# Kernel tuning notes

Hardware: AMD Instinct MI355X
Metric: run time of the kernel (lower is better)

The kernel has to match this reference:

```python
import jax, jax.numpy as jnp
import numpy as np

DIM = 1024
EXP = 4
B, S = 4, 4096


def setup_inputs() -> dict:
    key = jax.random.key(0)
    ks = jax.random.split(key, 20)
    d, h = DIM, DIM * EXP
    sc = 1.0 / np.sqrt(d)
    inp = {
        "x": jax.random.normal(ks[0], (B, S, d), dtype=jnp.float32),
        # attention linears, stored [in, out] so y = x @ W + b
        "wq": jax.random.normal(ks[1], (d, d), jnp.float32) * sc,
        "bq": jnp.zeros((d,), jnp.float32),
        "wk": jax.random.normal(ks[2], (d, d), jnp.float32) * sc,
        "bk": jnp.zeros((d,), jnp.float32),
        "wv": jax.random.normal(ks[3], (d, d), jnp.float32) * sc,
        "bv": jnp.zeros((d,), jnp.float32),
        "wo": jax.random.normal(ks[4], (d, d), jnp.float32) * sc,
        "bo": jnp.zeros((d,), jnp.float32),
        # FFN
        "w1": jax.random.normal(ks[5], (d, h), jnp.float32) * sc,
        "b1": jnp.zeros((h,), jnp.float32),
        "w2": jax.random.normal(ks[6], (h, d), jnp.float32) * (1.0 / np.sqrt(h)),
        "b2": jnp.zeros((d,), jnp.float32),
        # LayerNorms
        "g1": jnp.ones((d,), jnp.float32),
        "beta1": jnp.zeros((d,), jnp.float32),
        "g2": jnp.ones((d,), jnp.float32),
        "beta2": jnp.zeros((d,), jnp.float32),
    }
    return inp


def _layernorm(x, g, b, eps=1e-5):
    mu = jnp.mean(x, axis=-1, keepdims=True)
    var = jnp.mean(jnp.square(x - mu), axis=-1, keepdims=True)
    return (x - mu) * jax.lax.rsqrt(var + eps) * g + b


def _block(x, wq, bq, wk, bk, wv, bv, wo, bo, w1, b1, w2, b2, g1, beta1, g2, beta2):
    d = x.shape[-1]
    # attention sub-block (single head, full [B,S,S] scores as in source)
    h = _layernorm(x, g1, beta1)
    q = h @ wq + bq
    k = h @ wk + bk
    v = h @ wv + bv
    scores = jnp.einsum("bsd,btd->bst", q, k) / jnp.sqrt(jnp.asarray(d, x.dtype))
    attn = jax.nn.softmax(scores, axis=-1)
    a = jnp.einsum("bst,btd->bsd", attn, v) @ wo + bo
    x = x + a
    # FFN sub-block (exact GELU, matching torch nn.GELU default)
    h2 = _layernorm(x, g2, beta2)
    f = jax.nn.gelu(h2 @ w1 + b1, approximate=False) @ w2 + b2
    return x + f


def reference(x, wq, bq, wk, bk, wv, bv, wo, bo, w1, b1, w2, b2, g1, beta1, g2, beta2):
    return _block(x, wq, bq, wk, bk, wv, bv, wo, bo, w1, b1, w2, b2, g1, beta1, g2, beta2)
```

## Files before the change

kernel.cpp:

```cpp
#include <hip/hip_runtime.h>
#include <hip/hip_bf16.h>
#include <cstdint>

typedef __bf16 bf16;
typedef __bf16 bf16x8 __attribute__((ext_vector_type(8)));
typedef __bf16 bf16x4 __attribute__((ext_vector_type(4)));
typedef float f32x4 __attribute__((ext_vector_type(4)));

#define DEV __device__ __forceinline__

DEV float wred_sum(float v) {
#pragma unroll
  for (int off = 32; off > 0; off >>= 1) v += __shfl_xor(v, off, 64);
  return v;
}
DEV float wred_max(float v) {
#pragma unroll
  for (int off = 32; off > 0; off >>= 1) v = fmaxf(v, __shfl_xor(v, off, 64));
  return v;
}

__global__ void convT_kernel(const float* __restrict__ in, bf16* __restrict__ out,
                             int K, int N) {
  __shared__ float t[32][33];
  const int n0 = blockIdx.x * 32, k0 = blockIdx.y * 32;
  const int tx = threadIdx.x & 31, ty = threadIdx.x >> 5;
#pragma unroll
  for (int i = 0; i < 4; i++)
    t[ty + 8 * i][tx] = in[(long)(k0 + ty + 8 * i) * N + n0 + tx];
  __syncthreads();
#pragma unroll
  for (int i = 0; i < 4; i++)
    out[(long)(n0 + ty + 8 * i) * K + k0 + tx] = (bf16)t[tx][ty + 8 * i];
}

__global__ void transpose_bf16(const bf16* __restrict__ in, bf16* __restrict__ out,
                               int ldin, int ldout) {
  __shared__ bf16 t[32][33];
  const int c0 = blockIdx.x * 32, r0 = blockIdx.y * 32;
  const int tx = threadIdx.x & 31, ty = threadIdx.x >> 5;
#pragma unroll
  for (int i = 0; i < 4; i++)
    t[ty + 8 * i][tx] = in[(long)(r0 + ty + 8 * i) * ldin + c0 + tx];
  __syncthreads();
#pragma unroll
  for (int i = 0; i < 4; i++)
    out[(long)(c0 + ty + 8 * i) * ldout + r0 + tx] = t[tx][ty + 8 * i];
}

__global__ void ln_bf16_kernel(const float* __restrict__ x, const float* __restrict__ g,
                               const float* __restrict__ be, bf16* __restrict__ out) {
  const long row = blockIdx.x;
  const int tid = threadIdx.x;
  const float4 v = ((const float4*)(x + row * 1024))[tid];
  float s = v.x + v.y + v.z + v.w;
  float s2 = v.x * v.x + v.y * v.y + v.z * v.z + v.w * v.w;
  __shared__ float rs_[4], rs2_[4];
  s = wred_sum(s);
  s2 = wred_sum(s2);
  const int wave = tid >> 6, lane = tid & 63;
  if (lane == 0) { rs_[wave] = s; rs2_[wave] = s2; }
  __syncthreads();
  s = rs_[0] + rs_[1] + rs_[2] + rs_[3];
  s2 = rs2_[0] + rs2_[1] + rs2_[2] + rs2_[3];
  const float mu = s * (1.0f / 1024.0f);
  const float var = s2 * (1.0f / 1024.0f) - mu * mu;
  const float rstd = rsqrtf(var + 1e-5f);
  const float4 gg = ((const float4*)g)[tid];
  const float4 bb = ((const float4*)be)[tid];
  bf16x4 o;
  o[0] = (bf16)((v.x - mu) * rstd * gg.x + bb.x);
  o[1] = (bf16)((v.y - mu) * rstd * gg.y + bb.y);
  o[2] = (bf16)((v.z - mu) * rstd * gg.z + bb.z);
  o[3] = (bf16)((v.w - mu) * rstd * gg.w + bb.w);
  *(bf16x4*)(out + row * 1024 + tid * 4) = o;
}

__global__ void softmax_kernel(bf16* __restrict__ p) {
  const long row = blockIdx.x;
  bf16* pr = p + row * 4096;
  const int tid = threadIdx.x;
  bf16x8 a = *(const bf16x8*)(pr + tid * 16);
  bf16x8 b = *(const bf16x8*)(pr + tid * 16 + 8);
  float v[16];
#pragma unroll
  for (int i = 0; i < 8; i++) { v[i] = (float)a[i]; v[8 + i] = (float)b[i]; }
  float mx = -1e30f;
#pragma unroll
  for (int i = 0; i < 16; i++) mx = fmaxf(mx, v[i]);
  __shared__ float red1[4], red2[4];
  mx = wred_max(mx);
  const int wave = tid >> 6, lane = tid & 63;
  if (lane == 0) red1[wave] = mx;
  __syncthreads();
  mx = fmaxf(fmaxf(red1[0], red1[1]), fmaxf(red1[2], red1[3]));
  float s = 0.0f;
#pragma unroll
  for (int i = 0; i < 16; i++) { v[i] = __expf(v[i] - mx); s += v[i]; }
  s = wred_sum(s);
  if (lane == 0) red2[wave] = s;
  __syncthreads();
  s = red2[0] + red2[1] + red2[2] + red2[3];
  const float inv = 1.0f / s;
#pragma unroll
  for (int i = 0; i < 8; i++) { a[i] = (bf16)(v[i] * inv); b[i] = (bf16)(v[8 + i] * inv); }
  *(bf16x8*)(pr + tid * 16) = a;
  *(bf16x8*)(pr + tid * 16 + 8) = b;
}

enum { EPI_BF16 = 0, EPI_QKV = 1, EPI_GELU = 2, EPI_F32RES = 3 };

DEV void stage16(const bf16* g, bf16* l) {
  __builtin_amdgcn_global_load_lds((const __attribute__((address_space(1))) void*)g,
                                   (__attribute__((address_space(3))) void*)l, 16, 0, 0);
}

template <int EPI>
__global__ __launch_bounds__(256, 2)
void gemm128(const bf16* __restrict__ A, const bf16* __restrict__ B,
             const float* __restrict__ bias, const float* __restrict__ resid,
             void* Cout, int M, int N, int K,
             int lda, int ldb, int ldc, float alpha) {
  __shared__ __align__(16) bf16 sA[2 * 8192];
  __shared__ __align__(16) bf16 sB[2 * 8192];
  const int tid = threadIdx.x;
  const int lane = tid & 63;
  const int wid = tid >> 6;
  const int q = lane >> 4, r16 = lane & 15;
  const int wr = wid >> 1, wc = wid & 1;
  const long m0 = (long)blockIdx.y * 128;
  const long n0 = (long)blockIdx.x * 128;
  const int srow = tid >> 3;
  const int gcol = ((tid & 7) ^ (srow & 7)) * 8;
  const long lda32 = (long)lda * 32, ldb32 = (long)ldb * 32;
  const bf16* Ag = A + (m0 + srow) * (long)lda + gcol;
  const bf16* Bg = B + (n0 + srow) * (long)ldb + gcol;
  const int NT = K >> 6;
  const int swz = r16 * 64 + ((q ^ (r16 & 7)) * 8);
  const int abase = wr * 4096 + swz;
  const int bbase = wc * 4096 + swz;
  f32x4 acc[4][4] = {};

#pragma unroll
  for (int blk = 0; blk < 4; ++blk) {
    stage16(Ag + blk * lda32, sA + tid * 8 + blk * 2048);
    stage16(Bg + blk * ldb32, sB + tid * 8 + blk * 2048);
  }
  asm volatile("s_waitcnt vmcnt(0)" ::: "memory");
  __builtin_amdgcn_sched_barrier(0);
  __builtin_amdgcn_s_barrier();
  __builtin_amdgcn_sched_barrier(0);

  for (int t = 0; t < NT; ++t) {
    const int bx = (t & 1) * 8192;
    const int nbx = 8192 - bx;
    if (t + 1 < NT) {
      const bf16* Agn = Ag + (t + 1) * 64;
      const bf16* Bgn = Bg + (t + 1) * 64;
#pragma unroll
      for (int blk = 0; blk < 4; ++blk) {
        stage16(Agn + blk * lda32, sA + nbx + tid * 8 + blk * 2048);
        stage16(Bgn + blk * ldb32, sB + nbx + tid * 8 + blk * 2048);
      }
    }
    const bf16* sAb = sA + bx;
    const bf16* sBb = sB + bx;
    bf16x8 a0[4], a1[4], b0[4], b1[4];
#pragma unroll
    for (int i = 0; i < 4; ++i) {
      a0[i] = *(const bf16x8*)(sAb + (abase + i * 1024));
      a1[i] = *(const bf16x8*)(sAb + ((abase + i * 1024) ^ 32));
      b0[i] = *(const bf16x8*)(sBb + (bbase + i * 1024));
      b1[i] = *(const bf16x8*)(sBb + ((bbase + i * 1024) ^ 32));
    }
#pragma unroll
    for (int i = 0; i < 4; ++i)
#pragma unroll
      for (int j = 0; j < 4; ++j) {
        acc[i][j] = __builtin_amdgcn_mfma_f32_16x16x32_bf16(b0[j], a0[i], acc[i][j], 0, 0, 0);
        acc[i][j] = __builtin_amdgcn_mfma_f32_16x16x32_bf16(b1[j], a1[i], acc[i][j], 0, 0, 0);
      }
    if (t + 1 < NT) {
      asm volatile("s_waitcnt vmcnt(0)" ::: "memory");
      __builtin_amdgcn_sched_barrier(0);
      __builtin_amdgcn_s_barrier();
      __builtin_amdgcn_sched_barrier(0);
    }
  }

#pragma unroll
  for (int i = 0; i < 4; ++i) {
    const long row = m0 + wr * 64 + i * 16 + r16;
#pragma unroll
    for (int j = 0; j < 4; ++j) {
      const int ncol = (int)n0 + wc * 64 + j * 16 + q * 4;
      float4 b4 = make_float4(0.f, 0.f, 0.f, 0.f);
      if (bias != nullptr) b4 = *(const float4*)(bias + ncol);
      float v0 = acc[i][j][0] * alpha + b4.x;
      float v1 = acc[i][j][1] * alpha + b4.y;
      float v2 = acc[i][j][2] * alpha + b4.z;
      float v3 = acc[i][j][3] * alpha + b4.w;
      if (EPI == EPI_F32RES) {
        const long idx = row * (long)ldc + ncol;
        const float4 rr = *(const float4*)(resid + idx);
        const float4 o = make_float4(v0 + rr.x, v1 + rr.y, v2 + rr.z, v3 + rr.w);
        *(float4*)((float*)Cout + idx) = o;
      } else {
        bf16x4 o;
        o[0] = (bf16)v0; o[1] = (bf16)v1; o[2] = (bf16)v2; o[3] = (bf16)v3;
        *(bf16x4*)((bf16*)Cout + row * (long)ldc + ncol) = o;
      }
    }
  }
}

template <int EPI>
__global__ __launch_bounds__(512, 2)
void gemm256(const bf16* __restrict__ A, const bf16* __restrict__ B,
             const float* __restrict__ bias, const float* bias2, const float* bias3,
             const float* resid, void* Cout, int M, int N, int K,
             int lda, int ldb, int ldc, float alpha) {
  extern __shared__ __align__(16) char smem[];
  bf16* sA = (bf16*)smem;
  bf16* sB = sA + 32768;
  const int tid = threadIdx.x;
  const int lane = tid & 63;
  const int wid = tid >> 6;
  const int q = lane >> 4, r16 = lane & 15;
  const int wr = wid >> 2, wc = wid & 3;
  const long m0 = (long)blockIdx.y * 256;
  const long n0 = (long)blockIdx.x * 256;
  const int srow = tid >> 3;
  const int gcol = ((tid & 7) ^ (srow & 7)) * 8;
  const long lda64 = (long)lda * 64, ldb64 = (long)ldb * 64;
  const bf16* AgT = A + (m0 + srow) * (long)lda + gcol;
  const bf16* BgT = B + (n0 + srow) * (long)ldb + gcol;
  bf16* lA = sA + tid * 8;
  bf16* lB = sB + tid * 8;
  const int NT = K >> 6;
  const int swz = r16 * 64 + ((q ^ (r16 & 7)) * 8);
  const int abase = wr * 8192 + swz;
  const int bbase = (wc >> 1) * 8192 + (wc & 1) * 4096 + swz;

  f32x4 acc[8][4] = {};

  stage16(BgT,             lB);
  stage16(BgT + ldb64,     lB + 4096);
  stage16(BgT + 2 * ldb64, lB + 8192);
  stage16(BgT + 3 * ldb64, lB + 12288);
  stage16(AgT,             lA);
  stage16(AgT + lda64,     lA + 4096);
  stage16(AgT + 2 * lda64, lA + 8192);
  stage16(AgT + 3 * lda64, lA + 12288);
  if (NT > 1) {
    stage16(BgT + 64,             lB + 16384);
    stage16(BgT + 64 + ldb64,     lB + 16384 + 4096);
    stage16(BgT + 64 + 2 * ldb64, lB + 16384 + 8192);
    stage16(BgT + 64 + 3 * ldb64, lB + 16384 + 12288);
    asm volatile("s_waitcnt vmcnt(4)" ::: "memory");
  } else {
    asm volatile("s_waitcnt vmcnt(0)" ::: "memory");
  }
  __builtin_amdgcn_sched_barrier(0);
  __builtin_amdgcn_s_barrier();
  __builtin_amdgcn_sched_barrier(0);

  for (int t = 0; t < NT; ++t) {
    const int bx = (t & 1) * 16384;
    const int nbx = 16384 - bx;
    const bf16* sAb = sA + bx;
    const bf16* sBb = sB + bx;
    bf16x8 b0[4], b1[4];
#pragma unroll
    for (int p = 0; p < 4; ++p) {
      if (p == 0) {
#pragma unroll
        for (int n = 0; n < 4; ++n) {
          b0[n] = *(const bf16x8*)(sBb + (bbase + n * 1024));
          b1[n] = *(const bf16x8*)(sBb + ((bbase + n * 1024) ^ 32));
        }
      }
      const int ab = abase + p * 2048;
      const bf16x8 a00 = *(const bf16x8*)(sAb + ab);
      const bf16x8 a10 = *(const bf16x8*)(sAb + (ab ^ 32));
      const bf16x8 a01 = *(const bf16x8*)(sAb + (ab + 1024));
      const bf16x8 a11 = *(const bf16x8*)(sAb + ((ab + 1024) ^ 32));
      if (p == 0 && t + 1 < NT) {
        stage16(AgT + 64,         lA + nbx);
        stage16(AgT + 64 + lda64, lA + nbx + 4096);
      }
      if (p == 1 && t + 1 < NT) {
        stage16(AgT + 64 + 2 * lda64, lA + nbx + 8192);
        stage16(AgT + 64 + 3 * lda64, lA + nbx + 12288);
      }
      if (p == 2 && t + 2 < NT) {
        stage16(BgT + 128,         lB + bx);
        stage16(BgT + 128 + ldb64, lB + bx + 4096);
      }
      if (p == 3 && t + 2 < NT) {
        stage16(BgT + 128 + 2 * ldb64, lB + bx + 8192);
        stage16(BgT + 128 + 3 * ldb64, lB + bx + 12288);
      }
      __builtin_amdgcn_sched_barrier(0);
      __builtin_amdgcn_s_barrier();
      __builtin_amdgcn_sched_barrier(0);
      __builtin_amdgcn_s_setprio(1);
#pragma unroll
      for (int n = 0; n < 4; ++n) {
        acc[2 * p][n]     = __builtin_amdgcn_mfma_f32_16x16x32_bf16(b0[n], a00, acc[2 * p][n], 0, 0, 0);
        acc[2 * p][n]     = __builtin_amdgcn_mfma_f32_16x16x32_bf16(b1[n], a10, acc[2 * p][n], 0, 0, 0);
        acc[2 * p + 1][n] = __builtin_amdgcn_mfma_f32_16x16x32_bf16(b0[n], a01, acc[2 * p + 1][n], 0, 0, 0);
        acc[2 * p + 1][n] = __builtin_amdgcn_mfma_f32_16x16x32_bf16(b1[n], a11, acc[2 * p + 1][n], 0, 0, 0);
      }
      __builtin_amdgcn_s_setprio(0);
      if (p == 3) {
        if (t + 2 < NT)      asm volatile("s_waitcnt vmcnt(4)" ::: "memory");
        else if (t + 1 < NT) asm volatile("s_waitcnt vmcnt(0)" ::: "memory");
      }
      __builtin_amdgcn_sched_barrier(0);
      __builtin_amdgcn_s_barrier();
      __builtin_amdgcn_sched_barrier(0);
    }
    AgT += 64;
    BgT += 64;
  }

#pragma unroll
  for (int m = 0; m < 8; ++m) {
    const long row = m0 + wr * 128 + m * 16 + r16;
#pragma unroll
    for (int n = 0; n < 4; ++n) {
      const int ncol = (int)n0 + wc * 64 + n * 16 + q * 4;
      float4 b4 = make_float4(0.f, 0.f, 0.f, 0.f);
      if (EPI == EPI_QKV) {
        const int band = ncol >> 10;
        const float* bsel = band == 0 ? bias : (band == 1 ? bias2 : bias3);
        b4 = *(const float4*)(bsel + (ncol & 1023));
      } else if (bias != nullptr) {
        b4 = *(const float4*)(bias + ncol);
      }
      float v0 = acc[m][n][0] * alpha + b4.x;
      float v1 = acc[m][n][1] * alpha + b4.y;
      float v2 = acc[m][n][2] * alpha + b4.z;
      float v3 = acc[m][n][3] * alpha + b4.w;
      if (EPI == EPI_GELU) {
        v0 = 0.5f * v0 * (1.0f + erff(v0 * 0.70710678118654752f));
        v1 = 0.5f * v1 * (1.0f + erff(v1 * 0.70710678118654752f));
        v2 = 0.5f * v2 * (1.0f + erff(v2 * 0.70710678118654752f));
        v3 = 0.5f * v3 * (1.0f + erff(v3 * 0.70710678118654752f));
      }
      if (EPI == EPI_F32RES) {
        const long idx = row * (long)ldc + ncol;
        const float4 rr = *(const float4*)(resid + idx);
        const float4 o = make_float4(v0 + rr.x, v1 + rr.y, v2 + rr.z, v3 + rr.w);
        *(float4*)((float*)Cout + idx) = o;
      } else {
        bf16x4 o;
        o[0] = (bf16)v0; o[1] = (bf16)v1; o[2] = (bf16)v2; o[3] = (bf16)v3;
        *(bf16x4*)((bf16*)Cout + row * (long)ldc + ncol) = o;
      }
    }
  }
}

extern "C" void kernel_launch(void* const* d_in, const int* in_sizes, int n_in,
                              void* d_out, int out_size, void* d_ws, size_t ws_size,
                              hipStream_t stream) {
  const float* x  = (const float*)d_in[0];
  const float* wq = (const float*)d_in[1];
  const float* bq = (const float*)d_in[2];
  const float* wk = (const float*)d_in[3];
  const float* bk = (const float*)d_in[4];
  const float* wv = (const float*)d_in[5];
  const float* bv = (const float*)d_in[6];
  const float* wo = (const float*)d_in[7];
  const float* bo = (const float*)d_in[8];
  const float* w1 = (const float*)d_in[9];
  const float* b1 = (const float*)d_in[10];
  const float* w2 = (const float*)d_in[11];
  const float* b2 = (const float*)d_in[12];
  const float* g1 = (const float*)d_in[13];
  const float* be1 = (const float*)d_in[14];
  const float* g2 = (const float*)d_in[15];
  const float* be2 = (const float*)d_in[16];

  static int attr_done = 0;
  if (!attr_done) {
    attr_done = 1;
    hipFuncSetAttribute(reinterpret_cast<const void*>(&gemm256<EPI_QKV>),
                        hipFuncAttributeMaxDynamicSharedMemorySize, 131072);
    hipFuncSetAttribute(reinterpret_cast<const void*>(&gemm256<EPI_BF16>),
                        hipFuncAttributeMaxDynamicSharedMemorySize, 131072);
    hipFuncSetAttribute(reinterpret_cast<const void*>(&gemm256<EPI_GELU>),
                        hipFuncAttributeMaxDynamicSharedMemorySize, 131072);
    hipFuncSetAttribute(reinterpret_cast<const void*>(&gemm256<EPI_F32RES>),
                        hipFuncAttributeMaxDynamicSharedMemorySize, 131072);
  }

  const long MB = 1 << 20;
  char* ws = (char*)d_ws;
  char* ob = (char*)d_out;
  bf16* WQKV = (bf16*)(ws + 0 * MB);
  bf16* WO   = (bf16*)(ws + 6 * MB);
  bf16* W1   = (bf16*)(ws + 8 * MB);
  bf16* W2   = (bf16*)(ws + 16 * MB);
  bf16* H    = (bf16*)(ws + 24 * MB);
  bf16* P    = (bf16*)(ob + 0 * MB);
  bf16* QKVb = (bf16*)(ob + 32 * MB);
  bf16* Vt   = (bf16*)(ob + 56 * MB);
  float* OUT = (float*)d_out;
  const dim3 blk(256);
  const dim3 blk512(512);
  const size_t SMEM = 131072;

  convT_kernel<<<dim3(32, 32), blk, 0, stream>>>(wq, WQKV, 1024, 1024);
  convT_kernel<<<dim3(32, 32), blk, 0, stream>>>(wk, WQKV + 1024 * 1024, 1024, 1024);
  convT_kernel<<<dim3(32, 32), blk, 0, stream>>>(wv, WQKV + 2048 * 1024, 1024, 1024);
  convT_kernel<<<dim3(32, 32), blk, 0, stream>>>(wo, WO, 1024, 1024);
  convT_kernel<<<dim3(128, 32), blk, 0, stream>>>(w1, W1, 1024, 4096);
  convT_kernel<<<dim3(32, 128), blk, 0, stream>>>(w2, W2, 4096, 1024);
  ln_bf16_kernel<<<16384, blk, 0, stream>>>(x, g1, be1, H);
  for (int z = 0; z < 4; z++) {
    const long zo = (long)z * 4096 * 1024;
    gemm256<EPI_QKV><<<dim3(12, 16), blk512, SMEM, stream>>>(
        H + zo, WQKV, bq, bk, bv, nullptr, QKVb,
        4096, 3072, 1024, 1024, 1024, 3072, 1.0f);
    transpose_bf16<<<dim3(32, 128), blk, 0, stream>>>(QKVb + 2048, Vt, 3072, 4096);
    gemm256<EPI_BF16><<<dim3(16, 16), blk512, SMEM, stream>>>(
        QKVb, QKVb + 1024, nullptr, nullptr, nullptr, nullptr, P,
        4096, 4096, 1024, 3072, 3072, 4096, 1.0f / 32.0f);
    softmax_kernel<<<4096, blk, 0, stream>>>(P);
    gemm128<EPI_BF16><<<dim3(8, 32), blk, 0, stream>>>(
        P, Vt, nullptr, nullptr, H + zo,
        4096, 1024, 4096, 4096, 4096, 1024, 1.0f);
  }
  gemm256<EPI_F32RES><<<dim3(4, 64), blk512, SMEM, stream>>>(
      H, WO, bo, nullptr, nullptr, x, OUT,
      16384, 1024, 1024, 1024, 1024, 1024, 1.0f);
  bf16* H2m = (bf16*)(ws + 0 * MB);
  bf16* Fm  = (bf16*)(ws + 24 * MB);
  for (int mc = 0; mc < 4; mc++) {
    const long ro = (long)mc * 4096 * 1024;
    ln_bf16_kernel<<<4096, blk, 0, stream>>>(OUT + ro, g2, be2, H2m);
    gemm256<EPI_GELU><<<dim3(16, 16), blk512, SMEM, stream>>>(
        H2m, W1, b1, nullptr, nullptr, nullptr, Fm,
        4096, 4096, 1024, 1024, 1024, 4096, 1.0f);
    gemm128<EPI_F32RES><<<dim3(8, 32), blk, 0, stream>>>(
        Fm, W2, b2, OUT + ro, OUT + ro,
        4096, 1024, 4096, 4096, 4096, 1024, 1.0f);
  }
  (void)in_sizes; (void)n_in; (void)out_size; (void)ws_size;
}
```

Before: 1.439 ms.

## Triple-buffer gemm128 LDS pipeline and remap blocks across XCDs

The gemm128 kernel moves from a double-buffered to a triple-buffered LDS pipeline in dynamic shared memory. Tiles are prefetched two K-steps ahead, and partial vmcnt waits let global loads overlap more compute. The kernel also remaps the flat block index so that blocks dispatched round-robin to the same XCD get contiguous tiles, which is meant to improve L2 locality. The larger LDS footprint (96KB) and the dropped min-blocks launch bound may reduce occupancy to one block per CU.

```diff
diff --git a/kernel.cpp b/kernel.cpp
--- a/kernel.cpp
+++ b/kernel.cpp
@@ -116,20 +116,29 @@
 }
 
 template <int EPI>
-__global__ __launch_bounds__(256, 2)
+__global__ __launch_bounds__(256)
 void gemm128(const bf16* __restrict__ A, const bf16* __restrict__ B,
              const float* __restrict__ bias, const float* __restrict__ resid,
              void* Cout, int M, int N, int K,
              int lda, int ldb, int ldc, float alpha) {
-  __shared__ __align__(16) bf16 sA[2 * 8192];
-  __shared__ __align__(16) bf16 sB[2 * 8192];
+  extern __shared__ __align__(16) char smem[];
+  bf16* sA = (bf16*)smem;
+  bf16* sB = sA + 3 * 8192;
+  int flat = (int)(blockIdx.y * gridDim.x + blockIdx.x);
+  {
+    const int nwg = (int)(gridDim.x * gridDim.y);
+    const int qq = nwg >> 3, rr = nwg & 7;
+    const int xcd = flat & 7, idx = flat >> 3;
+    flat = (xcd < rr ? xcd * (qq + 1) : rr * (qq + 1) + (xcd - rr) * qq) + idx;
+  }
+  const int bix = flat % (int)gridDim.x, biy = flat / (int)gridDim.x;
   const int tid = threadIdx.x;
   const int lane = tid & 63;
   const int wid = tid >> 6;
   const int q = lane >> 4, r16 = lane & 15;
   const int wr = wid >> 1, wc = wid & 1;
-  const long m0 = (long)blockIdx.y * 128;
-  const long n0 = (long)blockIdx.x * 128;
+  const long m0 = (long)biy * 128;
+  const long n0 = (long)bix * 128;
   const int srow = tid >> 3;
   const int gcol = ((tid & 7) ^ (srow & 7)) * 8;
   const long lda32 = (long)lda * 32, ldb32 = (long)ldb * 32;
@@ -146,21 +155,29 @@
     stage16(Ag + blk * lda32, sA + tid * 8 + blk * 2048);
     stage16(Bg + blk * ldb32, sB + tid * 8 + blk * 2048);
   }
-  asm volatile("s_waitcnt vmcnt(0)" ::: "memory");
+  if (NT > 1) {
+#pragma unroll
+    for (int blk = 0; blk < 4; ++blk) {
+      stage16(Ag + 64 + blk * lda32, sA + 8192 + tid * 8 + blk * 2048);
+      stage16(Bg + 64 + blk * ldb32, sB + 8192 + tid * 8 + blk * 2048);
+    }
+    asm volatile("s_waitcnt vmcnt(8)" ::: "memory");
+  } else {
+    asm volatile("s_waitcnt vmcnt(0)" ::: "memory");
+  }
   __builtin_amdgcn_sched_barrier(0);
   __builtin_amdgcn_s_barrier();
   __builtin_amdgcn_sched_barrier(0);
 
+  int bx = 0, bs = 16384;
   for (int t = 0; t < NT; ++t) {
-    const int bx = (t & 1) * 8192;
-    const int nbx = 8192 - bx;
-    if (t + 1 < NT) {
-      const bf16* Agn = Ag + (t + 1) * 64;
-      const bf16* Bgn = Bg + (t + 1) * 64;
+    if (t + 2 < NT) {
+      const bf16* Agn = Ag + (t + 2) * 64;
+      const bf16* Bgn = Bg + (t + 2) * 64;
 #pragma unroll
       for (int blk = 0; blk < 4; ++blk) {
-        stage16(Agn + blk * lda32, sA + nbx + tid * 8 + blk * 2048);
-        stage16(Bgn + blk * ldb32, sB + nbx + tid * 8 + blk * 2048);
+        stage16(Agn + blk * lda32, sA + bs + tid * 8 + blk * 2048);
+        stage16(Bgn + blk * ldb32, sB + bs + tid * 8 + blk * 2048);
       }
     }
     const bf16* sAb = sA + bx;
@@ -180,12 +197,18 @@
         acc[i][j] = __builtin_amdgcn_mfma_f32_16x16x32_bf16(b0[j], a0[i], acc[i][j], 0, 0, 0);
         acc[i][j] = __builtin_amdgcn_mfma_f32_16x16x32_bf16(b1[j], a1[i], acc[i][j], 0, 0, 0);
       }
+    if (t + 2 < NT) {
+      asm volatile("s_waitcnt vmcnt(8)" ::: "memory");
+    } else if (t + 1 < NT) {
+      asm volatile("s_waitcnt vmcnt(0)" ::: "memory");
+    }
     if (t + 1 < NT) {
-      asm volatile("s_waitcnt vmcnt(0)" ::: "memory");
       __builtin_amdgcn_sched_barrier(0);
       __builtin_amdgcn_s_barrier();
       __builtin_amdgcn_sched_barrier(0);
     }
+    bx += 8192; if (bx == 24576) bx = 0;
+    bs += 8192; if (bs == 24576) bs = 0;
   }
 
 #pragma unroll
@@ -395,6 +418,10 @@
                         hipFuncAttributeMaxDynamicSharedMemorySize, 131072);
     hipFuncSetAttribute(reinterpret_cast<const void*>(&gemm256<EPI_F32RES>),
                         hipFuncAttributeMaxDynamicSharedMemorySize, 131072);
+    hipFuncSetAttribute(reinterpret_cast<const void*>(&gemm128<EPI_BF16>),
+                        hipFuncAttributeMaxDynamicSharedMemorySize, 98304);
+    hipFuncSetAttribute(reinterpret_cast<const void*>(&gemm128<EPI_F32RES>),
+                        hipFuncAttributeMaxDynamicSharedMemorySize, 98304);
   }
 
   const long MB = 1 << 20;
@@ -412,6 +439,7 @@
   const dim3 blk(256);
   const dim3 blk512(512);
   const size_t SMEM = 131072;
+  const size_t SMEM128 = 98304;
 
   convT_kernel<<<dim3(32, 32), blk, 0, stream>>>(wq, WQKV, 1024, 1024);
   convT_kernel<<<dim3(32, 32), blk, 0, stream>>>(wk, WQKV + 1024 * 1024, 1024, 1024);
@@ -430,7 +458,7 @@
         QKVb, QKVb + 1024, nullptr, nullptr, nullptr, nullptr, P,
         4096, 4096, 1024, 3072, 3072, 4096, 1.0f / 32.0f);
     softmax_kernel<<<4096, blk, 0, stream>>>(P);
-    gemm128<EPI_BF16><<<dim3(8, 32), blk, 0, stream>>>(
+    gemm128<EPI_BF16><<<dim3(8, 32), blk, SMEM128, stream>>>(
         P, Vt, nullptr, nullptr, H + zo,
         4096, 1024, 4096, 4096, 4096, 1024, 1.0f);
   }
@@ -445,7 +473,7 @@
     gemm256<EPI_GELU><<<dim3(16, 16), blk512, SMEM, stream>>>(
         H2m, W1, b1, nullptr, nullptr, nullptr, Fm,
         4096, 4096, 1024, 1024, 1024, 4096, 1.0f);
-    gemm128<EPI_F32RES><<<dim3(8, 32), blk, 0, stream>>>(
+    gemm128<EPI_F32RES><<<dim3(8, 32), blk, SMEM128, stream>>>(
         Fm, W2, b2, OUT + ro, OUT + ro,
         4096, 1024, 4096, 4096, 4096, 1024, 1.0f);
   }
```

Result: faster. 1.248 ms (-13.2%).
